# Kernel optimization log

Hardware: AMD Instinct MI355X
Metric: run time of the kernel (lower is better)

The kernel has to match this reference:

```python
import jax, jax.numpy as jnp
import numpy as np
import math

N_HEAD = 16
ROPE_BASE = 10000.0


def _rope(xh):
    # xh: [B, H, T, D]; rotate full head dim using half-split (GPT-NeoX style)
    B, H, T, D = xh.shape
    theta = 1.0 / (ROPE_BASE ** (jnp.arange(0, D, 2, dtype=jnp.float32) / D))  # [D/2]
    idx_theta = jnp.arange(T, dtype=jnp.float32)[:, None] * theta[None, :]      # [T, D/2]
    idx_theta2 = jnp.concatenate([idx_theta, idx_theta], axis=1)                 # [T, D]
    cos = jnp.cos(idx_theta2)[None, None]                                        # [1,1,T,D]
    sin = jnp.sin(idx_theta2)[None, None]
    d2 = D // 2
    neg_half = jnp.concatenate([-xh[..., d2:], xh[..., :d2]], axis=-1)
    return xh * cos + neg_half * sin


def setup_inputs() -> dict:
    key = jax.random.key(0)
    k1, k2, k3 = jax.random.split(key, 3)
    B, T, C = 2, 2048, 2048
    x = jax.random.normal(k1, (B, T, C), dtype=jnp.float32)
    w_attn = jax.random.normal(k2, (C, 3 * C), dtype=jnp.float32) * (1.0 / math.sqrt(C))
    w_proj = jax.random.normal(k3, (C, C), dtype=jnp.float32) * (1.0 / math.sqrt(C))
    return {"x": x, "w_attn": w_attn, "w_proj": w_proj}


def reference(x, w_attn, w_proj):
    B, T, C = x.shape
    H = N_HEAD
    D = C // H
    qkv = x @ w_attn                                   # [B,T,3C]
    q, k, v = jnp.split(qkv, 3, axis=-1)
    # [B,T,C] -> [B,H,T,D]
    to_heads = lambda t: t.reshape(B, T, H, D).transpose(0, 2, 1, 3)
    q, k, v = to_heads(q), to_heads(k), to_heads(v)
    q = _rope(q)
    k = _rope(k)
    att = jnp.einsum('bhqd,bhkd->bhqk', q, k) * (1.0 / math.sqrt(D))
    causal = jnp.tril(jnp.ones((T, T), dtype=bool))
    att = jnp.where(causal[None, None], att, -jnp.inf)
    att = jax.nn.softmax(att, axis=-1)
    y = jnp.einsum('bhqk,bhkd->bhqd', att, v)          # [B,H,T,D]
    y = y.transpose(0, 2, 1, 3).reshape(B, T, C)
    return y @ w_proj
```

## Files before the change

### kernel.cpp

```cpp
#include <hip/hip_runtime.h>
#include <hip/hip_bf16.h>
#include <math.h>

typedef __bf16 bf16;
typedef __bf16 bf16x8 __attribute__((ext_vector_type(8)));
typedef float f32x4 __attribute__((ext_vector_type(4)));
typedef float f32x16 __attribute__((ext_vector_type(16)));
typedef unsigned int u32x2 __attribute__((ext_vector_type(2)));
typedef unsigned int u32x4 __attribute__((ext_vector_type(4)));

#define MFMA16(a, b, c) __builtin_amdgcn_mfma_f32_16x16x32_bf16((a), (b), (c), 0, 0, 0)
#define MFMA32(a, b, c) __builtin_amdgcn_mfma_f32_32x32x16_bf16((a), (b), (c), 0, 0, 0)

static constexpr int Bsz = 2, Tsz = 2048, Csz = 2048, Hn = 16, Dh = 128;
static constexpr float ATTN_SCALE = 0.08838834764831845f;

__device__ __forceinline__ void gld16(const void* src, void* dst) {
    __builtin_amdgcn_global_load_lds((__attribute__((address_space(1))) void*)src,
                                     (__attribute__((address_space(3))) void*)dst,
                                     16, 0, 0);
}

__device__ __forceinline__ unsigned cvt_pk_bf16(float lo, float hi) {
    unsigned r;
    asm("v_cvt_pk_bf16_f32 %0, %1, %2" : "=v"(r) : "v"(lo), "v"(hi));
    return r;
}

__device__ __forceinline__ bf16x8 make_pfrag(float p0, float p1, float p2, float p3,
                                             float p4, float p5, float p6, float p7) {
    unsigned a0 = cvt_pk_bf16(p0, p1), a1 = cvt_pk_bf16(p2, p3);
    unsigned b0 = cvt_pk_bf16(p4, p5), b1 = cvt_pk_bf16(p6, p7);
    asm volatile("v_permlane32_swap_b32 %0, %1" : "+v"(a0), "+v"(b0));
    asm volatile("v_permlane32_swap_b32 %0, %1" : "+v"(a1), "+v"(b1));
    u32x4 w = {a0, a1, b0, b1};
    return __builtin_bit_cast(bf16x8, w);
}

__global__ __launch_bounds__(256) void cast_x_kernel(const float* __restrict__ x,
                                                     bf16* __restrict__ o, int n8) {
    int i = blockIdx.x * 256 + threadIdx.x;
    if (i >= n8) return;
    const float4* x4 = (const float4*)x;
    float4 a = x4[2 * i], b = x4[2 * i + 1];
    bf16x8 v;
    v[0] = (bf16)a.x; v[1] = (bf16)a.y; v[2] = (bf16)a.z; v[3] = (bf16)a.w;
    v[4] = (bf16)b.x; v[5] = (bf16)b.y; v[6] = (bf16)b.z; v[7] = (bf16)b.w;
    ((bf16x8*)o)[i] = v;
}

template <typename TIN>
__global__ __launch_bounds__(256) void transpose_cast_kernel(const TIN* __restrict__ in,
                                                             bf16* __restrict__ out,
                                                             int R, int Cc) {
    __shared__ float tile[64][65];
    const int tx = threadIdx.x, ty = threadIdx.y;
    in  += (size_t)blockIdx.z * R * Cc;
    out += (size_t)blockIdx.z * R * Cc;
    const int c0 = blockIdx.x * 64, r0 = blockIdx.y * 64;
#pragma unroll
    for (int j = 0; j < 16; ++j) {
        int rr = ty + j * 4;
        tile[rr][tx] = (float)in[(size_t)(r0 + rr) * Cc + c0 + tx];
    }
    __syncthreads();
#pragma unroll
    for (int j = 0; j < 16; ++j) {
        int cc = ty + j * 4;
        out[(size_t)(c0 + cc) * R + r0 + tx] = (bf16)tile[tx][cc];
    }
}

__global__ __launch_bounds__(256) void cossin_kernel(float2* __restrict__ cs) {
    int idx = blockIdx.x * 256 + threadIdx.x;
    int t = idx >> 6, i = idx & 63;
    float theta = 1.0f / powf(10000.0f, (float)(2 * i) / 128.0f);
    float ang = (float)t * theta;
    cs[idx] = make_float2(cosf(ang), sinf(ang));
}

template <int MODE>
__global__ __launch_bounds__(256)
void gemm128_bt(const bf16* __restrict__ A, const bf16* __restrict__ Bt,
                float* __restrict__ Cf,
                bf16* __restrict__ Oq, bf16* __restrict__ Ok, bf16* __restrict__ Ov,
                const float2* __restrict__ cs,
                int M, int N, int K) {
    __shared__ bf16 sA[128 * 64];
    __shared__ bf16 sB[128 * 64];
    const int tid = threadIdx.x;
    const int lane = tid & 63, wv = tid >> 6;
    const int wr = wv >> 1, wc = wv & 1;
    const int lo16 = lane & 15, hi4 = lane >> 4;
    const int row0 = blockIdx.y << 7, col0 = blockIdx.x << 7;

    f32x4 acc[4][4] = {};

    const int nkt = K >> 6;
    for (int kt = 0; kt < nkt; ++kt) {
        const int kbase = kt << 6;
#pragma unroll
        for (int c = 0; c < 4; ++c) {
            const int o16 = (c << 8) + tid;
            const int row = o16 >> 3, u = o16 & 7;
            const int colel = kbase + ((u ^ (row & 7)) << 3);
            gld16(A  + (size_t)(row0 + row) * K + colel,
                  (char*)sA + (((c << 8) + (wv << 6)) << 4));
            gld16(Bt + (size_t)(col0 + row) * K + colel,
                  (char*)sB + (((c << 8) + (wv << 6)) << 4));
        }
        __syncthreads();
#pragma unroll
        for (int ks = 0; ks < 2; ++ks) {
            bf16x8 af[4], bfv[4];
#pragma unroll
            for (int mi = 0; mi < 4; ++mi) {
                const int ar = (wr << 6) + (mi << 4) + lo16;
                af[mi] = *(const bf16x8*)((const char*)sA + ar * 128 +
                          (((ks << 6) + (hi4 << 4)) ^ ((ar & 7) << 4)));
            }
#pragma unroll
            for (int ni = 0; ni < 4; ++ni) {
                const int bc = (wc << 4) + (ni << 5) + lo16;
                bfv[ni] = *(const bf16x8*)((const char*)sB + bc * 128 +
                           (((ks << 6) + (hi4 << 4)) ^ ((bc & 7) << 4)));
            }
#pragma unroll
            for (int mi = 0; mi < 4; ++mi)
#pragma unroll
                for (int ni = 0; ni < 4; ++ni)
                    acc[mi][ni] = MFMA16(af[mi], bfv[ni], acc[mi][ni]);
        }
        __syncthreads();
    }

    if (MODE == 0) {
#pragma unroll
        for (int mi = 0; mi < 4; ++mi)
#pragma unroll
            for (int r = 0; r < 4; ++r) {
                const int gm = row0 + (wr << 6) + (mi << 4) + (hi4 << 2) + r;
                float* crow = Cf + (size_t)gm * N + col0 + (wc << 4) + lo16;
#pragma unroll
                for (int ni = 0; ni < 4; ++ni)
                    crow[ni << 5] = acc[mi][ni][r];
            }
    } else {
        const int seg = col0 >> 11;
        const int h = (col0 >> 7) & 15;
        if (seg < 2) {
            bf16* dst0 = (seg == 0) ? Oq : Ok;
            const float qs = (seg == 0) ? ATTN_SCALE : 1.0f;
#pragma unroll
            for (int mi = 0; mi < 4; ++mi)
#pragma unroll
                for (int r = 0; r < 4; ++r) {
                    const int gm = row0 + (wr << 6) + (mi << 4) + (hi4 << 2) + r;
                    const int b = gm >> 11, t = gm & 2047;
                    bf16* drow = dst0 + ((((size_t)b * Hn + h) * Tsz + t) << 7);
#pragma unroll
                    for (int ni = 0; ni < 2; ++ni) {
                        const int dlo = (wc << 4) + (ni << 5) + lo16;
                        const float2 csv = cs[t * 64 + dlo];
                        const float vlo = acc[mi][ni][r];
                        const float vhi = acc[mi][ni + 2][r];
                        drow[dlo]      = (bf16)((vlo * csv.x - vhi * csv.y) * qs);
                        drow[dlo + 64] = (bf16)((vhi * csv.x + vlo * csv.y) * qs);
                    }
                }
        } else {
#pragma unroll
            for (int mi = 0; mi < 4; ++mi)
#pragma unroll
                for (int r = 0; r < 4; ++r) {
                    const int gm = row0 + (wr << 6) + (mi << 4) + (hi4 << 2) + r;
                    const int b = gm >> 11, t = gm & 2047;
                    bf16* drow = Ov + ((((size_t)b * Hn + h) * Tsz + t) << 7);
#pragma unroll
                    for (int ni = 0; ni < 4; ++ni)
                        drow[(wc << 4) + (ni << 5) + lo16] = (bf16)acc[mi][ni][r];
                }
        }
    }
}

__device__ __forceinline__ void stage_tile(const bf16* __restrict__ Kb,
                                           const bf16* __restrict__ Vtb,
                                           bf16* sKc, bf16* sVc, int k0, int tid) {
#pragma unroll
    for (int c = 0; c < 4; ++c) {
        const int off = (c << 12) + (tid << 4);
        const int row = off >> 8, u = (off >> 4) & 15;
        gld16(Kb + (size_t)(k0 + row) * Dh + ((u ^ (row & 7)) << 3), (char*)sKc + off);
        const int dv = off >> 7, uv = (off >> 4) & 7;
        gld16(Vtb + (size_t)dv * Tsz + k0 + ((uv ^ (dv & 7)) << 3), (char*)sVc + off);
    }
}

__global__ __launch_bounds__(256, 2)
void attn_kernel(const bf16* __restrict__ Q, const bf16* __restrict__ K,
                 const bf16* __restrict__ Vt, bf16* __restrict__ Y) {
    __shared__ bf16 sK[2][64 * 128];
    __shared__ bf16 sV[2][128 * 64];
    const int tid = threadIdx.x, lane = tid & 63, wv = tid >> 6;
    const int lo32 = lane & 31, hl = lane >> 5;

    const int i = blockIdx.x;
    const int g = i >> 5;
    const int bh = i & 31;
    const int t = (i < 256) ? (15 - g) : (g - 8);
    const int b = bh >> 4, h = bh & 15;

    const int q0 = t << 7;
    const int q0w = q0 + (wv << 5);
    const int qg = q0w + lo32;

    const bf16* Kb  = K  + (size_t)bh * (Tsz * Dh);
    const bf16* Vtb = Vt + (size_t)bh * (Tsz * Dh);
    const bf16* Qp  = Q  + (size_t)bh * (Tsz * Dh) + (size_t)qg * Dh;

    bf16x8 qf[8];
#pragma unroll
    for (int kc = 0; kc < 8; ++kc)
        qf[kc] = *(const bf16x8*)(Qp + (kc << 4) + (hl << 3));

    float m = -1e30f, lsum = 0.f;
    f32x16 o[4] = {};

    const int nt_block = 2 * t + 2;
    const int nt_warp = ((q0w + 31) >> 6) + 1;

    stage_tile(Kb, Vtb, &sK[0][0], &sV[0][0], 0, tid);

    int cur = 0;
    for (int kt = 0; kt < nt_block; ++kt) {
        __syncthreads();
        if (kt + 1 < nt_block)
            stage_tile(Kb, Vtb, &sK[cur ^ 1][0], &sV[cur ^ 1][0], (kt + 1) << 6, tid);
        if (kt < nt_warp) {
            const int k0 = kt << 6;
            const bf16* kbuf = &sK[cur][0];
            const bf16* vbuf = &sV[cur][0];
            f32x16 s0 = {}, s1 = {};
            const int swk = lo32 & 7;
            __builtin_amdgcn_s_setprio(1);
#pragma unroll
            for (int kc = 0; kc < 8; ++kc) {
                bf16x8 kf0 = *(const bf16x8*)((const char*)kbuf + lo32 * 256 +
                              ((((kc << 1) + hl) ^ swk) << 4));
                s0 = MFMA32(kf0, qf[kc], s0);
                bf16x8 kf1 = *(const bf16x8*)((const char*)kbuf + (32 + lo32) * 256 +
                              ((((kc << 1) + hl) ^ swk) << 4));
                s1 = MFMA32(kf1, qf[kc], s1);
            }
            __builtin_amdgcn_s_setprio(0);

            const bool bnd = (k0 + 63 > q0w);
            if (bnd) {
#pragma unroll
                for (int r = 0; r < 16; ++r) {
                    const int kl = (r & 3) + ((r >> 2) << 3) + (hl << 2);
                    if (k0 + kl > qg)      s0[r] = -1e30f;
                    if (k0 + 32 + kl > qg) s1[r] = -1e30f;
                }
            }
            float pm = s0[0];
#pragma unroll
            for (int r = 1; r < 16; ++r) pm = fmaxf(pm, s0[r]);
#pragma unroll
            for (int r = 0; r < 16; ++r) pm = fmaxf(pm, s1[r]);
            pm = fmaxf(pm, __shfl_xor(pm, 32));

            if (__any(pm > m + 8.0f)) {
                const float mn = fmaxf(m, pm);
                const float sc = __expf(m - mn);
                m = mn;
                lsum *= sc;
#pragma unroll
                for (int db = 0; db < 4; ++db)
#pragma unroll
                    for (int r = 0; r < 16; ++r) o[db][r] *= sc;
            }
            float rs = 0.f;
            if (bnd) {
#pragma unroll
                for (int r = 0; r < 16; ++r) {
                    float e0 = (s0[r] > -1e29f) ? __expf(s0[r] - m) : 0.f;
                    float e1 = (s1[r] > -1e29f) ? __expf(s1[r] - m) : 0.f;
                    s0[r] = e0; s1[r] = e1; rs += e0 + e1;
                }
            } else {
#pragma unroll
                for (int r = 0; r < 16; ++r) {
                    float e0 = __expf(s0[r] - m);
                    float e1 = __expf(s1[r] - m);
                    s0[r] = e0; s1[r] = e1; rs += e0 + e1;
                }
            }
            rs += __shfl_xor(rs, 32);
            lsum += rs;

            bf16x8 pb0 = make_pfrag(s0[0], s0[1], s0[2],  s0[3],  s0[4],  s0[5],  s0[6],  s0[7]);
            bf16x8 pb1 = make_pfrag(s0[8], s0[9], s0[10], s0[11], s0[12], s0[13], s0[14], s0[15]);
            bf16x8 pb2 = make_pfrag(s1[0], s1[1], s1[2],  s1[3],  s1[4],  s1[5],  s1[6],  s1[7]);
            bf16x8 pb3 = make_pfrag(s1[8], s1[9], s1[10], s1[11], s1[12], s1[13], s1[14], s1[15]);

            __builtin_amdgcn_s_setprio(1);
#pragma unroll
            for (int db = 0; db < 4; ++db) {
                const int rd = (db << 5) + lo32;
                const char* vrow = (const char*)vbuf + rd * 128;
                const int sw = rd & 7;
                bf16x8 v0 = *(const bf16x8*)(vrow + (((0 + hl) ^ sw) << 4));
                o[db] = MFMA32(v0, pb0, o[db]);
                bf16x8 v1 = *(const bf16x8*)(vrow + (((2 + hl) ^ sw) << 4));
                o[db] = MFMA32(v1, pb1, o[db]);
                bf16x8 v2 = *(const bf16x8*)(vrow + (((4 + hl) ^ sw) << 4));
                o[db] = MFMA32(v2, pb2, o[db]);
                bf16x8 v3 = *(const bf16x8*)(vrow + (((6 + hl) ^ sw) << 4));
                o[db] = MFMA32(v3, pb3, o[db]);
            }
            __builtin_amdgcn_s_setprio(0);
        }
        cur ^= 1;
    }

    const float inv = 1.0f / lsum;
    const size_t rowoff = ((size_t)b * Tsz + qg) * (size_t)Csz + (size_t)h * 128;
#pragma unroll
    for (int db = 0; db < 4; ++db)
#pragma unroll
        for (int gg = 0; gg < 4; ++gg) {
            unsigned w0 = cvt_pk_bf16(o[db][4 * gg + 0] * inv, o[db][4 * gg + 1] * inv);
            unsigned w1 = cvt_pk_bf16(o[db][4 * gg + 2] * inv, o[db][4 * gg + 3] * inv);
            u32x2 w = {w0, w1};
            *(u32x2*)(Y + rowoff + (db << 5) + (gg << 3) + (hl << 2)) = w;
        }
}

extern "C" void kernel_launch(void* const* d_in, const int* in_sizes, int n_in,
                              void* d_out, int out_size, void* d_ws, size_t ws_size,
                              hipStream_t stream) {
    const float* x      = (const float*)d_in[0];
    const float* w_attn = (const float*)d_in[1];
    const float* w_proj = (const float*)d_in[2];
    float* out = (float*)d_out;

    char* ws = (char*)d_ws;
    bf16* Xb  = (bf16*)(ws);
    bf16* Wat = (bf16*)(ws + 16777216);
    bf16* Wpt = (bf16*)(ws + 41943040);
    bf16* Qr  = (bf16*)(ws + 50331648);
    bf16* Kr  = (bf16*)(ws + 67108864);
    bf16* Vb  = (bf16*)(ws + 83886080);
    bf16* Vt  = (bf16*)(ws + 100663296);
    bf16* Yb  = (bf16*)(ws + 117440512);
    float2* cs = (float2*)(ws + 134217728);

    cast_x_kernel<<<4096, 256, 0, stream>>>(x, Xb, (Bsz * Tsz * Csz) / 8);
    transpose_cast_kernel<float><<<dim3(96, 32, 1), dim3(64, 4), 0, stream>>>(w_attn, Wat, 2048, 6144);
    transpose_cast_kernel<float><<<dim3(32, 32, 1), dim3(64, 4), 0, stream>>>(w_proj, Wpt, 2048, 2048);
    cossin_kernel<<<512, 256, 0, stream>>>(cs);

    gemm128_bt<1><<<dim3(48, 32), 256, 0, stream>>>(Xb, Wat, nullptr, Qr, Kr, Vb, cs,
                                                    4096, 6144, 2048);
    transpose_cast_kernel<bf16><<<dim3(2, 32, 32), dim3(64, 4), 0, stream>>>(Vb, Vt, 2048, 128);

    attn_kernel<<<dim3(512), 256, 0, stream>>>(Qr, Kr, Vt, Yb);

    gemm128_bt<0><<<dim3(16, 32), 256, 0, stream>>>(Yb, Wpt, out, nullptr, nullptr, nullptr,
                                                    nullptr, 4096, 2048, 2048);
}
```

Before: 263.5 us.

## Add 256x256 double-buffered pipelined GEMM for QKV projection with RoPE epilogue

Replaces the 128x128 QKV GEMM with a 512-thread, 256x256-tile kernel. It double-buffers LDS with async global-to-LDS loads interleaved across four MFMA sub-phases, and uses explicit waitcnt, setprio and a block-index swizzle to group blocks for L2 reuse. The aim is to hide global load latency and raise MFMA utilisation and data reuse for the largest GEMM. The trade-offs are 128 KB of LDS per block, which limits occupancy, and hand-tuned barrier and waitcnt ordering that is fragile to get right.

```diff
diff --git a/kernel.cpp b/kernel.cpp
--- a/kernel.cpp
+++ b/kernel.cpp
@@ -79,13 +79,207 @@
     cs[idx] = make_float2(cosf(ang), sinf(ang));
 }
 
-template <int MODE>
+__global__ __launch_bounds__(512, 2)
+void gemm256_qkv(const bf16* __restrict__ A, const bf16* __restrict__ Bt,
+                 bf16* __restrict__ Oq, bf16* __restrict__ Ok, bf16* __restrict__ Ov,
+                 const float2* __restrict__ cs, int K) {
+    __shared__ bf16 sA[2][256 * 64];
+    __shared__ bf16 sB[2][256 * 64];
+    const int tid = threadIdx.x, lane = tid & 63, wid = tid >> 6;
+    const int wm = wid >> 2, wn = wid & 3;
+    const int lo16 = lane & 15, hi4 = lane >> 4;
+
+    const int cpx = gridDim.x >> 3;
+    const int swz = (blockIdx.x & 7) * cpx + (blockIdx.x >> 3);
+    const int by = swz & 15;
+    const int bx = swz >> 4;
+    const int row0 = by << 8, col0 = bx << 8;
+
+    const int srow = tid >> 3;
+    const int swzoff = (((tid & 7) ^ ((tid >> 3) & 7)) << 3);
+    const bf16* srcA = A  + (size_t)(row0 + srow) * K + swzoff;
+    const bf16* srcB = Bt + (size_t)(col0 + srow) * K + swzoff;
+    const size_t K64 = (size_t)K * 64, K128 = (size_t)K * 128;
+    char* const ldsA = (char*)&sA[0][0];
+    char* const ldsB = (char*)&sB[0][0];
+    const int wuo = wid << 10;
+
+    auto issueA0 = [&](int c, int kt) {
+        const bf16* s = srcA + (size_t)kt * 64;
+        gld16(s,        ldsA + (c << 15) + 0     + wuo);
+        gld16(s + K128, ldsA + (c << 15) + 16384 + wuo);
+    };
+    auto issueA1 = [&](int c, int kt) {
+        const bf16* s = srcA + (size_t)kt * 64 + K64;
+        gld16(s,        ldsA + (c << 15) + 8192  + wuo);
+        gld16(s + K128, ldsA + (c << 15) + 24576 + wuo);
+    };
+    auto issueBlo = [&](int c, int kt) {
+        const bf16* s = srcB + (size_t)kt * 64;
+        gld16(s,       ldsB + (c << 15) + 0    + wuo);
+        gld16(s + K64, ldsB + (c << 15) + 8192 + wuo);
+    };
+    auto issueBhi = [&](int c, int kt) {
+        const bf16* s = srcB + (size_t)kt * 64 + K128;
+        gld16(s,       ldsB + (c << 15) + 16384 + wuo);
+        gld16(s + K64, ldsB + (c << 15) + 24576 + wuo);
+    };
+    auto ldF = [&](const char* buf, int row, int ks) {
+        return *(const bf16x8*)(buf + row * 128 + ((((ks << 2) + hi4) ^ (row & 7)) << 4));
+    };
+
+    const int arow = (wm << 7) + lo16;
+    const int brow = (wn << 4) + lo16;
+
+    f32x4 acc[8][4] = {};
+    const int nkt = K >> 6;
+
+    issueBhi(0, 0); issueA1(0, 0); issueA0(0, 0); issueBlo(0, 0);
+    if (nkt > 1) {
+        issueA0(1, 1); issueBlo(1, 1);
+        asm volatile("s_waitcnt vmcnt(4)" ::: "memory");
+    } else {
+        asm volatile("s_waitcnt vmcnt(0)" ::: "memory");
+    }
+    __builtin_amdgcn_s_barrier();
+
+    for (int kt = 0; kt < nkt; ++kt) {
+        const int c = kt & 1;
+        const char* bufA = ldsA + (c << 15);
+        const char* bufB = ldsB + (c << 15);
+        bf16x8 af[4][2], bq[2][2];
+#pragma unroll
+        for (int i = 0; i < 4; ++i) {
+            af[i][0] = ldF(bufA, arow + (i << 4), 0);
+            af[i][1] = ldF(bufA, arow + (i << 4), 1);
+        }
+#pragma unroll
+        for (int j = 0; j < 2; ++j) {
+            bq[j][0] = ldF(bufB, brow + (j << 6), 0);
+            bq[j][1] = ldF(bufB, brow + (j << 6), 1);
+        }
+        if (kt + 1 < nkt) issueBhi(c ^ 1, kt + 1);
+        __builtin_amdgcn_s_barrier();
+        asm volatile("s_waitcnt lgkmcnt(0)" ::: "memory");
+        __builtin_amdgcn_sched_barrier(0);
+        __builtin_amdgcn_s_setprio(1);
+#pragma unroll
+        for (int ks = 0; ks < 2; ++ks)
+#pragma unroll
+            for (int i = 0; i < 4; ++i)
+#pragma unroll
+                for (int j = 0; j < 2; ++j)
+                    acc[i][j] = MFMA16(af[i][ks], bq[j][ks], acc[i][j]);
+        __builtin_amdgcn_s_setprio(0);
+        __builtin_amdgcn_s_barrier();
+#pragma unroll
+        for (int j = 0; j < 2; ++j) {
+            bq[j][0] = ldF(bufB, brow + ((j + 2) << 6), 0);
+            bq[j][1] = ldF(bufB, brow + ((j + 2) << 6), 1);
+        }
+        if (kt + 1 < nkt) issueA1(c ^ 1, kt + 1);
+        __builtin_amdgcn_s_barrier();
+        asm volatile("s_waitcnt lgkmcnt(0)" ::: "memory");
+        __builtin_amdgcn_sched_barrier(0);
+        __builtin_amdgcn_s_setprio(1);
+#pragma unroll
+        for (int ks = 0; ks < 2; ++ks)
+#pragma unroll
+            for (int i = 0; i < 4; ++i)
+#pragma unroll
+                for (int j = 0; j < 2; ++j)
+                    acc[i][j + 2] = MFMA16(af[i][ks], bq[j][ks], acc[i][j + 2]);
+        __builtin_amdgcn_s_setprio(0);
+        __builtin_amdgcn_s_barrier();
+#pragma unroll
+        for (int i = 0; i < 4; ++i) {
+            af[i][0] = ldF(bufA, arow + 64 + (i << 4), 0);
+            af[i][1] = ldF(bufA, arow + 64 + (i << 4), 1);
+        }
+#pragma unroll
+        for (int j = 0; j < 2; ++j) {
+            bq[j][0] = ldF(bufB, brow + (j << 6), 0);
+            bq[j][1] = ldF(bufB, brow + (j << 6), 1);
+        }
+        if (kt + 2 < nkt) issueA0(c, kt + 2);
+        __builtin_amdgcn_s_barrier();
+        asm volatile("s_waitcnt lgkmcnt(0)" ::: "memory");
+        __builtin_amdgcn_sched_barrier(0);
+        __builtin_amdgcn_s_setprio(1);
+#pragma unroll
+        for (int ks = 0; ks < 2; ++ks)
+#pragma unroll
+            for (int i = 0; i < 4; ++i)
+#pragma unroll
+                for (int j = 0; j < 2; ++j)
+                    acc[i + 4][j] = MFMA16(af[i][ks], bq[j][ks], acc[i + 4][j]);
+        __builtin_amdgcn_s_setprio(0);
+        __builtin_amdgcn_s_barrier();
+#pragma unroll
+        for (int j = 0; j < 2; ++j) {
+            bq[j][0] = ldF(bufB, brow + ((j + 2) << 6), 0);
+            bq[j][1] = ldF(bufB, brow + ((j + 2) << 6), 1);
+        }
+        if (kt + 2 < nkt) issueBlo(c, kt + 2);
+        __builtin_amdgcn_s_barrier();
+        asm volatile("s_waitcnt lgkmcnt(0)" ::: "memory");
+        __builtin_amdgcn_sched_barrier(0);
+        __builtin_amdgcn_s_setprio(1);
+#pragma unroll
+        for (int ks = 0; ks < 2; ++ks)
+#pragma unroll
+            for (int i = 0; i < 4; ++i)
+#pragma unroll
+                for (int j = 0; j < 2; ++j)
+                    acc[i + 4][j + 2] = MFMA16(af[i][ks], bq[j][ks], acc[i + 4][j + 2]);
+        __builtin_amdgcn_s_setprio(0);
+        if (kt + 2 < nkt) asm volatile("s_waitcnt vmcnt(4)" ::: "memory");
+        else              asm volatile("s_waitcnt vmcnt(0)" ::: "memory");
+        __builtin_amdgcn_s_barrier();
+    }
+
+    const int seg = col0 >> 11;
+    const int hb = (col0 >> 7) & 15;
+    if (seg < 2) {
+        bf16* dst0 = (seg == 0) ? Oq : Ok;
+        const float qs = (seg == 0) ? ATTN_SCALE : 1.0f;
+        const int d = (wn << 4) + lo16;
+#pragma unroll
+        for (int mi = 0; mi < 8; ++mi)
+#pragma unroll
+            for (int r = 0; r < 4; ++r) {
+                const int gm = row0 + (wm << 7) + (mi << 4) + (hi4 << 2) + r;
+                const int b = gm >> 11, t = gm & 2047;
+                const float2 csv = cs[t * 64 + d];
+#pragma unroll
+                for (int np = 0; np < 2; ++np) {
+                    bf16* drow = dst0 + ((((size_t)b * Hn + hb + np) * Tsz + t) << 7);
+                    const float vlo = acc[mi][2 * np][r];
+                    const float vhi = acc[mi][2 * np + 1][r];
+                    drow[d]      = (bf16)((vlo * csv.x - vhi * csv.y) * qs);
+                    drow[d + 64] = (bf16)((vhi * csv.x + vlo * csv.y) * qs);
+                }
+            }
+    } else {
+        const int d0 = (wn << 4) + lo16;
+#pragma unroll
+        for (int mi = 0; mi < 8; ++mi)
+#pragma unroll
+            for (int r = 0; r < 4; ++r) {
+                const int gm = row0 + (wm << 7) + (mi << 4) + (hi4 << 2) + r;
+                const int b = gm >> 11, t = gm & 2047;
+#pragma unroll
+                for (int ni = 0; ni < 4; ++ni) {
+                    bf16* drow = Ov + ((((size_t)b * Hn + hb + (ni >> 1)) * Tsz + t) << 7);
+                    drow[d0 + ((ni & 1) << 6)] = (bf16)acc[mi][ni][r];
+                }
+            }
+    }
+}
+
 __global__ __launch_bounds__(256)
 void gemm128_bt(const bf16* __restrict__ A, const bf16* __restrict__ Bt,
-                float* __restrict__ Cf,
-                bf16* __restrict__ Oq, bf16* __restrict__ Ok, bf16* __restrict__ Ov,
-                const float2* __restrict__ cs,
-                int M, int N, int K) {
+                float* __restrict__ Cf, int M, int N, int K) {
     __shared__ bf16 sA[128 * 64];
     __shared__ bf16 sB[128 * 64];
     const int tid = threadIdx.x;
@@ -134,54 +328,16 @@
         __syncthreads();
     }
 
-    if (MODE == 0) {
-#pragma unroll
-        for (int mi = 0; mi < 4; ++mi)
-#pragma unroll
-            for (int r = 0; r < 4; ++r) {
-                const int gm = row0 + (wr << 6) + (mi << 4) + (hi4 << 2) + r;
-                float* crow = Cf + (size_t)gm * N + col0 + (wc << 4) + lo16;
-#pragma unroll
-                for (int ni = 0; ni < 4; ++ni)
-                    crow[ni << 5] = acc[mi][ni][r];
-            }
-    } else {
-        const int seg = col0 >> 11;
-        const int h = (col0 >> 7) & 15;
-        if (seg < 2) {
-            bf16* dst0 = (seg == 0) ? Oq : Ok;
-            const float qs = (seg == 0) ? ATTN_SCALE : 1.0f;
-#pragma unroll
-            for (int mi = 0; mi < 4; ++mi)
-#pragma unroll
-                for (int r = 0; r < 4; ++r) {
-                    const int gm = row0 + (wr << 6) + (mi << 4) + (hi4 << 2) + r;
-                    const int b = gm >> 11, t = gm & 2047;
-                    bf16* drow = dst0 + ((((size_t)b * Hn + h) * Tsz + t) << 7);
-#pragma unroll
-                    for (int ni = 0; ni < 2; ++ni) {
-                        const int dlo = (wc << 4) + (ni << 5) + lo16;
-                        const float2 csv = cs[t * 64 + dlo];
-                        const float vlo = acc[mi][ni][r];
-                        const float vhi = acc[mi][ni + 2][r];
-                        drow[dlo]      = (bf16)((vlo * csv.x - vhi * csv.y) * qs);
-                        drow[dlo + 64] = (bf16)((vhi * csv.x + vlo * csv.y) * qs);
-                    }
-                }
-        } else {
-#pragma unroll
-            for (int mi = 0; mi < 4; ++mi)
-#pragma unroll
-                for (int r = 0; r < 4; ++r) {
-                    const int gm = row0 + (wr << 6) + (mi << 4) + (hi4 << 2) + r;
-                    const int b = gm >> 11, t = gm & 2047;
-                    bf16* drow = Ov + ((((size_t)b * Hn + h) * Tsz + t) << 7);
-#pragma unroll
-                    for (int ni = 0; ni < 4; ++ni)
-                        drow[(wc << 4) + (ni << 5) + lo16] = (bf16)acc[mi][ni][r];
-                }
-        }
-    }
+#pragma unroll
+    for (int mi = 0; mi < 4; ++mi)
+#pragma unroll
+        for (int r = 0; r < 4; ++r) {
+            const int gm = row0 + (wr << 6) + (mi << 4) + (hi4 << 2) + r;
+            float* crow = Cf + (size_t)gm * N + col0 + (wc << 4) + lo16;
+#pragma unroll
+            for (int ni = 0; ni < 4; ++ni)
+                crow[ni << 5] = acc[mi][ni][r];
+        }
 }
 
 __device__ __forceinline__ void stage_tile(const bf16* __restrict__ Kb,
@@ -362,12 +518,10 @@
     transpose_cast_kernel<float><<<dim3(32, 32, 1), dim3(64, 4), 0, stream>>>(w_proj, Wpt, 2048, 2048);
     cossin_kernel<<<512, 256, 0, stream>>>(cs);
 
-    gemm128_bt<1><<<dim3(48, 32), 256, 0, stream>>>(Xb, Wat, nullptr, Qr, Kr, Vb, cs,
-                                                    4096, 6144, 2048);
+    gemm256_qkv<<<384, 512, 0, stream>>>(Xb, Wat, Qr, Kr, Vb, cs, 2048);
     transpose_cast_kernel<bf16><<<dim3(2, 32, 32), dim3(64, 4), 0, stream>>>(Vb, Vt, 2048, 128);
 
     attn_kernel<<<dim3(512), 256, 0, stream>>>(Qr, Kr, Vt, Yb);
 
-    gemm128_bt<0><<<dim3(16, 32), 256, 0, stream>>>(Yb, Wpt, out, nullptr, nullptr, nullptr,
-                                                    nullptr, 4096, 2048, 2048);
-}
+    gemm128_bt<<<dim3(16, 32), 256, 0, stream>>>(Yb, Wpt, out, 4096, 2048, 2048);
+}
```

Measured after the change: 273.2 us. 3.7% more time.
